# Kernel tuning notes

Hardware: AMD Instinct MI355X
Metric: run time of the kernel (lower is better)

## Reference

```python
import jax, jax.numpy as jnp
import numpy as np

HEADS = 4
LN_EPS = 1e-5

def layernorm(x, w, b):
    m = x.mean(-1, keepdims=True)
    v = ((x - m) ** 2).mean(-1, keepdims=True)
    return (x - m) * jax.lax.rsqrt(v + LN_EPS) * w + b

def conv3d(x, w, b, pad, dil=1, groups=1):
    out = jax.lax.conv_general_dilated(
        x, w, (1, 1, 1), [(pad, pad)] * 3,
        rhs_dilation=(dil, dil, dil),
        dimension_numbers=('NCDHW', 'OIDHW', 'NCDHW'),
        feature_group_count=groups)
    return out + b[None, :, None, None, None]

def trilinear_gather(x_flat, pz, py, px, D, H, W):
    # x_flat: [B,C,S]; pz/py/px: [B,S] fractional sample coords, zero padding outside
    z0f, y0f, x0f = jnp.floor(pz), jnp.floor(py), jnp.floor(px)
    wz, wy, wx = pz - z0f, py - y0f, px - x0f
    z0, y0, x0 = z0f.astype(jnp.int32), y0f.astype(jnp.int32), x0f.astype(jnp.int32)
    acc = jnp.zeros_like(x_flat)
    for dz in (0, 1):
        for dy in (0, 1):
            for dx in (0, 1):
                iz, iy, ix = z0 + dz, y0 + dy, x0 + dx
                cw = (wz if dz else 1.0 - wz) * (wy if dy else 1.0 - wy) * (wx if dx else 1.0 - wx)
                valid = (iz >= 0) & (iz < D) & (iy >= 0) & (iy < H) & (ix >= 0) & (ix < W)
                idx = (jnp.clip(iz, 0, D - 1) * H + jnp.clip(iy, 0, H - 1)) * W + jnp.clip(ix, 0, W - 1)
                vals = jnp.take_along_axis(x_flat, idx[:, None, :], axis=2)
                acc = acc + vals * (cw * valid)[:, None, :]
    return acc

def deform_conv3d(x, off_w, off_b, w, b):
    # DeformConvPack: offsets from a regular 3x3x3 conv, then offset trilinear sampling + conv
    B, C, D, H, W = x.shape
    K = 27
    offsets = conv3d(x, off_w, off_b, 1).reshape(B, K, 3, D * H * W)
    gz, gy, gx = jnp.indices((D, H, W))
    bz = gz.reshape(-1).astype(x.dtype)[None]
    by = gy.reshape(-1).astype(x.dtype)[None]
    bx = gx.reshape(-1).astype(x.dtype)[None]
    x_flat = x.reshape(B, C, -1)
    O = w.shape[0]
    wk = w.reshape(O, C, K)
    out = jnp.zeros((B, O, D * H * W), x.dtype)
    for k in range(K):  # fixed 27 kernel taps
        kz, ky, kx = k // 9, (k // 3) % 3, k % 3
        pz = bz + (kz - 1) + offsets[:, k, 0]
        py = by + (ky - 1) + offsets[:, k, 1]
        px = bx + (kx - 1) + offsets[:, k, 2]
        samp = trilinear_gather(x_flat, pz, py, px, D, H, W)  # [B,C,S]
        out = out + jnp.einsum('bcs,oc->bos', samp, wk[:, :, k])
    out = out + b[None, :, None]
    return out.reshape(B, O, D, H, W)

def forward(x, temperature, qkv_w, norm_w, norm_b, proj1_w, proj1_b, conv0_w, conv0_b,
            convsp_w, convsp_b, off_w, off_b, dcn_w, dcn_b, conv1_w, conv1_b,
            proj2_w, proj2_b, norm2_w, norm2_b, out_w, out_b, H, W, D):
    B, N, C = x.shape
    hd = C // HEADS
    qkv = (x @ qkv_w.T).reshape(B, N, 3, HEADS, hd).transpose(2, 0, 3, 1, 4)  # [3,B,h,N,hd]
    q = qkv[0].transpose(0, 1, 3, 2)  # [B,h,hd,N]
    k = qkv[1].transpose(0, 1, 3, 2)
    v = qkv[2].transpose(0, 1, 3, 2)
    q = q / jnp.maximum(jnp.sqrt((q * q).sum(-1, keepdims=True)), 1e-12)
    k = k / jnp.maximum(jnp.sqrt((k * k).sum(-1, keepdims=True)), 1e-12)
    attn = jnp.einsum('bhcn,bhdn->bhcd', q, k) * temperature[None]
    attn = jax.nn.softmax(attn, axis=-1)
    x_ca = jnp.einsum('bhcd,bhdn->bhcn', attn, v).transpose(0, 3, 1, 2).reshape(B, N, C)
    x_ca = layernorm(x_ca, norm_w, norm_b)
    x5 = x_ca.transpose(0, 2, 1).reshape(B, C, H, W, D)
    shortcut = x5
    y = jnp.einsum('bcxyz,oc->boxyz', x5, proj1_w) + proj1_b[None, :, None, None, None]
    y = jax.nn.gelu(y, approximate=False)
    u = y
    a = conv3d(y, conv0_w, conv0_b, 2, 1, C)      # depthwise k=5 pad=2
    a = conv3d(a, convsp_w, convsp_b, 9, 3, C)    # depthwise k=7 pad=9 dil=3
    a = deform_conv3d(a, off_w, off_b, dcn_w, dcn_b)
    a = jnp.einsum('bcxyz,oc->boxyz', a, conv1_w) + conv1_b[None, :, None, None, None]
    y = u * a
    y = jnp.einsum('bcxyz,oc->boxyz', y, proj2_w) + proj2_b[None, :, None, None, None]
    y = y + shortcut
    x_sa = y.reshape(B, C, N).transpose(0, 2, 1)           # lka returns [B,N,C]
    x_sa = x_sa.reshape(B, C, N).transpose(0, 2, 1)        # faithful torch reshape-after-permute
    x_sa = layernorm(x_sa, norm2_w, norm2_b)
    return x_sa @ out_w.T + out_b

def setup_inputs():
    key = jax.random.key(0)
    ks = jax.random.split(key, 12)
    B, C, H, W, D = 2, 64, 32, 32, 32
    N = H * W * D
    s = 0.02
    return dict(
        x=jax.random.normal(ks[0], (B, N, C), jnp.float32),
        temperature=jnp.ones((HEADS, 1, 1), jnp.float32),
        qkv_w=jax.random.normal(ks[1], (3 * C, C), jnp.float32) * s,
        norm_w=jnp.ones((C,), jnp.float32), norm_b=jnp.zeros((C,), jnp.float32),
        proj1_w=jax.random.normal(ks[2], (C, C), jnp.float32) * s,
        proj1_b=jnp.zeros((C,), jnp.float32),
        conv0_w=jax.random.normal(ks[3], (C, 1, 5, 5, 5), jnp.float32) * s,
        conv0_b=jnp.zeros((C,), jnp.float32),
        convsp_w=jax.random.normal(ks[4], (C, 1, 7, 7, 7), jnp.float32) * s,
        convsp_b=jnp.zeros((C,), jnp.float32),
        off_w=jax.random.normal(ks[5], (81, C, 3, 3, 3), jnp.float32) * 0.01,
        off_b=jnp.zeros((81,), jnp.float32),
        dcn_w=jax.random.normal(ks[6], (C, C, 3, 3, 3), jnp.float32) * s,
        dcn_b=jnp.zeros((C,), jnp.float32),
        conv1_w=jax.random.normal(ks[7], (C, C), jnp.float32) * s,
        conv1_b=jnp.zeros((C,), jnp.float32),
        proj2_w=jax.random.normal(ks[8], (C, C), jnp.float32) * s,
        proj2_b=jnp.zeros((C,), jnp.float32),
        norm2_w=jnp.ones((C,), jnp.float32), norm2_b=jnp.zeros((C,), jnp.float32),
        out_w=jax.random.normal(ks[9], (C, C), jnp.float32) * s,
        out_b=jnp.zeros((C,), jnp.float32),
        B_in=B, C_in=C, H=H, W=W, D=D,
    )

def reference(x, temperature, qkv_w, norm_w, norm_b, proj1_w, proj1_b, conv0_w, conv0_b,
              convsp_w, convsp_b, off_w, off_b, dcn_w, dcn_b, conv1_w, conv1_b,
              proj2_w, proj2_b, norm2_w, norm2_b, out_w, out_b, B_in, C_in, H, W, D):
    return forward(x, temperature, qkv_w, norm_w, norm_b, proj1_w, proj1_b, conv0_w, conv0_b,
                   convsp_w, convsp_b, off_w, off_b, dcn_w, dcn_b, conv1_w, conv1_b,
                   proj2_w, proj2_b, norm2_w, norm2_b, out_w, out_b, H, W, D)
```

## Files before the change

### kernel.cpp

```cpp
#include <hip/hip_runtime.h>
#include <hip/hip_bf16.h>

#define S 32768
#define BUFN (2*64*32768)

typedef __bf16 v8bf __attribute__((ext_vector_type(8)));
typedef float v4f __attribute__((ext_vector_type(4)));
typedef int v4i __attribute__((ext_vector_type(4)));

__device__ __forceinline__ ushort f2b(float f) {
  union { float f; unsigned u; } v; v.f = f;
  unsigned r = (v.u + 0x7fffu + ((v.u >> 16) & 1u)) >> 16;
  return (ushort)r;
}
__device__ __forceinline__ float b2f(ushort h) {
  union { unsigned u; float f; } v; v.u = ((unsigned)h) << 16;
  return v.f;
}
__device__ __forceinline__ float u2f(unsigned u) {
  union { unsigned u; float f; } v; v.u = u;
  return v.f;
}

__global__ void k_wt(const float* __restrict__ offw, const float* __restrict__ dcnw,
                     const float* __restrict__ qkvw, const float* __restrict__ p1w,
                     ushort* __restrict__ wt_off16, ushort* __restrict__ wt_dcn16,
                     ushort* __restrict__ qkv16, ushort* __restrict__ p1w16) {
  int i = blockIdx.x*256 + threadIdx.x;
  if (i < 27*96*64) {
    int c = i & 63, o = (i >> 6) % 96, t = i / 6144;
    wt_off16[i] = (o < 81) ? f2b(offw[o*1728 + c*27 + t]) : (ushort)0;
  }
  if (i < 27*64*64) {
    int c = i & 63, o = (i >> 6) & 63, k = i >> 12;
    wt_dcn16[i] = f2b(dcnw[(o*64 + c)*27 + k]);
  }
  if (i < 12288) qkv16[i] = f2b(qkvw[i]);
  if (i < 4096)  p1w16[i] = f2b(p1w[i]);
}

__global__ __launch_bounds__(256) void k_qkv(const float* __restrict__ x,
    const ushort* __restrict__ qkvw16, float* __restrict__ q,
    float* __restrict__ k, float* __restrict__ v) {
  int bi = blockIdx.x;
  int b = bi >> 9, tile = bi & 511;
  int tid = threadIdx.x;
  int lane = tid & 63, wv = tid >> 6;
  int si = lane & 15, rq = lane >> 4, q8 = rq << 3;
  int s = (tile << 6) + (wv << 4) + si;
  const float* xr = x + ((size_t)(b*S + s) << 6);
  float4 t0 = *(const float4*)(xr + q8);
  float4 t1 = *(const float4*)(xr + q8 + 4);
  float4 t2 = *(const float4*)(xr + q8 + 32);
  float4 t3 = *(const float4*)(xr + q8 + 36);
  float f0[8] = {t0.x,t0.y,t0.z,t0.w,t1.x,t1.y,t1.z,t1.w};
  float f1[8] = {t2.x,t2.y,t2.z,t2.w,t3.x,t3.y,t3.z,t3.w};
  v4i d0, d1;
#pragma unroll
  for (int m = 0; m < 4; m++) {
    d0[m] = (int)((unsigned)f2b(f0[2*m]) | ((unsigned)f2b(f0[2*m+1]) << 16));
    d1[m] = (int)((unsigned)f2b(f1[2*m]) | ((unsigned)f2b(f1[2*m+1]) << 16));
  }
  v8bf b0 = __builtin_bit_cast(v8bf, d0);
  v8bf b1 = __builtin_bit_cast(v8bf, d1);
  v4f acc[12];
#pragma unroll
  for (int t = 0; t < 12; t++) acc[t] = (v4f){0.f,0.f,0.f,0.f};
#pragma unroll
  for (int t = 0; t < 12; t++) {
    const ushort* ap = qkvw16 + (((t<<4) + si) << 6) + q8;
    v8bf a0 = *(const v8bf*)ap;
    v8bf a1 = *(const v8bf*)(ap + 32);
    acc[t] = __builtin_amdgcn_mfma_f32_16x16x32_bf16(a0, b0, acc[t], 0,0,0);
    acc[t] = __builtin_amdgcn_mfma_f32_16x16x32_bf16(a1, b1, acc[t], 0,0,0);
  }
#pragma unroll
  for (int t = 0; t < 12; t++) {
    float* dst = (t < 4) ? q : (t < 8 ? k : v);
    int chb = (t & 3) << 4;
#pragma unroll
    for (int r = 0; r < 4; r++) {
      int ch = chb + rq*4 + r;
      dst[((size_t)(b*64 + ch))*S + s] = acc[t][r];
    }
  }
}

__global__ __launch_bounds__(256) void k_rownorm(const float* __restrict__ q,
    const float* __restrict__ k, float* __restrict__ inv) {
  int row = blockIdx.x;
  const float* p = (row < 128) ? (q + (size_t)row*S) : (k + (size_t)(row-128)*S);
  const float4* p4 = (const float4*)p;
  float ss = 0.f;
  for (int i = threadIdx.x; i < S/4; i += 256) {
    float4 t = p4[i];
    ss += t.x*t.x + t.y*t.y + t.z*t.z + t.w*t.w;
  }
  __shared__ float red[256];
  red[threadIdx.x] = ss; __syncthreads();
  for (int st = 128; st > 0; st >>= 1) {
    if (threadIdx.x < st) red[threadIdx.x] += red[threadIdx.x+st];
    __syncthreads();
  }
  if (threadIdx.x == 0) inv[row] = 1.0f / fmaxf(sqrtf(red[0]), 1e-12f);
}

__global__ __launch_bounds__(256) void k_gram(const float* __restrict__ q,
    const float* __restrict__ k, float* __restrict__ gram) {
  __shared__ float qt[16][65], kt[16][65];
  int bi = blockIdx.x;
  int b = bi >> 7, h = (bi >> 5) & 3, chunk = bi & 31;
  int c = threadIdx.x >> 4, d = threadIdx.x & 15;
  const float* qb = q + ((size_t)(b*64 + h*16))*S;
  const float* kb = k + ((size_t)(b*64 + h*16))*S;
  int lr = threadIdx.x >> 4, lc = (threadIdx.x & 15) * 4;
  float acc = 0.f;
  for (int n0 = chunk*1024; n0 < chunk*1024 + 1024; n0 += 64) {
    float4 tq = *(const float4*)(qb + (size_t)lr*S + n0 + lc);
    float4 tk = *(const float4*)(kb + (size_t)lr*S + n0 + lc);
    __syncthreads();
    qt[lr][lc]=tq.x; qt[lr][lc+1]=tq.y; qt[lr][lc+2]=tq.z; qt[lr][lc+3]=tq.w;
    kt[lr][lc]=tk.x; kt[lr][lc+1]=tk.y; kt[lr][lc+2]=tk.z; kt[lr][lc+3]=tk.w;
    __syncthreads();
#pragma unroll
    for (int nn = 0; nn < 64; nn++) acc += qt[c][nn]*kt[d][nn];
  }
  atomicAdd(&gram[((b*4+h)*16+c)*16 + d], acc);
}

__global__ __launch_bounds__(256) void k_xca_ln(const float* __restrict__ v,
    const float* __restrict__ gram, const float* __restrict__ inv,
    const float* __restrict__ temp,
    const float* __restrict__ nw, const float* __restrict__ nb,
    float* __restrict__ x5) {
  __shared__ float at[1024];
  __shared__ float wsh[64], bsh[64];
  int gid = blockIdx.x*256 + threadIdx.x;
  int b = gid >> 15, n = gid & (S-1);
  int tid = threadIdx.x;
  if (tid < 64) {
    int h = tid >> 4, c = tid & 15;
    float iq = inv[b*64 + h*16 + c];
    float tp = temp[h];
    float l[16], m = -1e30f;
#pragma unroll
    for (int d = 0; d < 16; d++) {
      float vv = gram[((b*4+h)*16+c)*16 + d] * iq * inv[128 + b*64 + h*16 + d] * tp;
      l[d] = vv; m = fmaxf(m, vv);
    }
    float s = 0.f;
#pragma unroll
    for (int d = 0; d < 16; d++) { l[d] = expf(l[d]-m); s += l[d]; }
    float is = 1.0f / s;
#pragma unroll
    for (int d = 0; d < 16; d++) at[(h*16+c)*16 + d] = l[d]*is;
  } else if (tid < 128) {
    wsh[tid-64] = nw[tid-64]; bsh[tid-64] = nb[tid-64];
  }
  __syncthreads();
  const float* vb = v + (size_t)b*64*S + n;
  float vv[64];
#pragma unroll
  for (int ch = 0; ch < 64; ch++) vv[ch] = vb[(size_t)ch*S];
  float xc[64];
#pragma unroll
  for (int h = 0; h < 4; h++)
#pragma unroll
    for (int cc = 0; cc < 16; cc++) {
      float a = 0.f;
#pragma unroll
      for (int d = 0; d < 16; d++) a += at[(h*16+cc)*16 + d] * vv[h*16+d];
      xc[h*16+cc] = a;
    }
  float mean = 0.f;
#pragma unroll
  for (int ch = 0; ch < 64; ch++) mean += xc[ch];
  mean *= (1.0f/64.0f);
  float var = 0.f;
#pragma unroll
  for (int ch = 0; ch < 64; ch++) { float d = xc[ch]-mean; var += d*d; }
  var *= (1.0f/64.0f);
  float rs = rsqrtf(var + 1e-5f);
  float* xb = x5 + (size_t)b*64*S + n;
#pragma unroll
  for (int ch = 0; ch < 64; ch++)
    xb[(size_t)ch*S] = (xc[ch]-mean)*rs*wsh[ch] + bsh[ch];
}

__global__ __launch_bounds__(256) void k_proj1(const float* __restrict__ x5,
    const ushort* __restrict__ p1w16, const float* __restrict__ bias, float* __restrict__ u) {
  int bi = blockIdx.x;
  int b = bi >> 9, tile = bi & 511;
  int tid = threadIdx.x;
  int lane = tid & 63, wv = tid >> 6;
  int si = lane & 15, rq = lane >> 4, q8 = rq << 3;
  int s = (tile << 6) + (wv << 4) + si;
  const float* xb = x5 + ((size_t)b << 21) + s;
  float f0[8], f1[8];
#pragma unroll
  for (int j = 0; j < 8; j++) {
    f0[j] = xb[(size_t)(q8 + j) << 15];
    f1[j] = xb[(size_t)(32 + q8 + j) << 15];
  }
  v4i d0, d1;
#pragma unroll
  for (int m = 0; m < 4; m++) {
    d0[m] = (int)((unsigned)f2b(f0[2*m]) | ((unsigned)f2b(f0[2*m+1]) << 16));
    d1[m] = (int)((unsigned)f2b(f1[2*m]) | ((unsigned)f2b(f1[2*m+1]) << 16));
  }
  v8bf b0 = __builtin_bit_cast(v8bf, d0);
  v8bf b1 = __builtin_bit_cast(v8bf, d1);
  v4f acc[4];
#pragma unroll
  for (int t = 0; t < 4; t++) acc[t] = (v4f){0.f,0.f,0.f,0.f};
#pragma unroll
  for (int t = 0; t < 4; t++) {
    const ushort* ap = p1w16 + (((t<<4) + si) << 6) + q8;
    v8bf a0 = *(const v8bf*)ap;
    v8bf a1 = *(const v8bf*)(ap + 32);
    acc[t] = __builtin_amdgcn_mfma_f32_16x16x32_bf16(a0, b0, acc[t], 0,0,0);
    acc[t] = __builtin_amdgcn_mfma_f32_16x16x32_bf16(a1, b1, acc[t], 0,0,0);
  }
  float* ub = u + ((size_t)b << 21) + s;
#pragma unroll
  for (int t = 0; t < 4; t++)
#pragma unroll
    for (int r = 0; r < 4; r++) {
      int ch = (t << 4) + rq*4 + r;
      float a = acc[t][r] + bias[ch];
      float g = 0.5f*a*(1.0f + erff(a*0.70710678118654752f));
      ub[(size_t)ch << 15] = g;
    }
}

__global__ __launch_bounds__(256) void k_conv0(const float* __restrict__ in,
    const float* __restrict__ w, const float* __restrict__ bias, ushort* __restrict__ out) {
  __shared__ ushort tile[5*32*40];
  __shared__ float wsh[128];
  int bi = blockIdx.x;
  int z = bi & 31, c = (bi >> 5) & 63, b = bi >> 11;
  const float* ib = in + ((size_t)(b*64+c) << 15);
  for (int i = threadIdx.x; i < 800; i += 256)
    ((int4*)tile)[i] = make_int4(0,0,0,0);
  if (threadIdx.x < 125) wsh[threadIdx.x] = w[c*125 + threadIdx.x];
  __syncthreads();
  for (int i = threadIdx.x; i < 5*1024; i += 256) {
    int dz = i >> 10, r = i & 1023;
    int zg = z + dz - 2;
    if (zg >= 0 && zg < 32)
      tile[(dz*32 + (r >> 5))*40 + (r & 31) + 2] = f2b(ib[zg*1024 + r]);
  }
  __syncthreads();
  int y = threadIdx.x >> 3, x0 = (threadIdx.x & 7) << 2;
  float bv = bias[c];
  float acc[4] = {bv, bv, bv, bv};
  for (int dz = 0; dz < 5; dz++) {
#pragma unroll
    for (int dy = 0; dy < 5; dy++) {
      int yy = y + dy - 2;
      if (yy < 0 || yy >= 32) continue;
      const float* wp = &wsh[(dz*5+dy)*5];
      float wreg[5];
#pragma unroll
      for (int dx = 0; dx < 5; dx++) wreg[dx] = wp[dx];
      const ushort* rp = &tile[(dz*32+yy)*40 + x0];
      int2 rl = *(const int2*)rp;
      int2 rh = *(const int2*)(rp + 4);
      float row[8];
      row[0]=u2f(((unsigned)rl.x)<<16); row[1]=u2f(rl.x & 0xffff0000u);
      row[2]=u2f(((unsigned)rl.y)<<16); row[3]=u2f(rl.y & 0xffff0000u);
      row[4]=u2f(((unsigned)rh.x)<<16); row[5]=u2f(rh.x & 0xffff0000u);
      row[6]=u2f(((unsigned)rh.y)<<16); row[7]=u2f(rh.y & 0xffff0000u);
#pragma unroll
      for (int dx = 0; dx < 5; dx++)
#pragma unroll
        for (int j = 0; j < 4; j++)
          acc[j] += wreg[dx] * row[dx+j];
    }
  }
  ushort* ob = out + ((size_t)(b*64+c) << 15) + z*1024 + y*32 + x0;
  unsigned p0 = (unsigned)f2b(acc[0]) | ((unsigned)f2b(acc[1]) << 16);
  unsigned p1 = (unsigned)f2b(acc[2]) | ((unsigned)f2b(acc[3]) << 16);
  *(int2*)ob = make_int2((int)p0, (int)p1);
}

__global__ __launch_bounds__(256) void k_convsp(const ushort* __restrict__ in,
    const float* __restrict__ w, const float* __restrict__ bias, ushort* __restrict__ out) {
  __shared__ ushort tile[7*32*56];
  __shared__ float wsh[344];
  int bi = blockIdx.x;
  int z = bi & 31, c = (bi >> 5) & 63, b = bi >> 11;
  const ushort* ib = in + ((size_t)(b*64+c) << 15);
  for (int i = threadIdx.x; i < 1568; i += 256)
    ((int4*)tile)[i] = make_int4(0,0,0,0);
  for (int i = threadIdx.x; i < 343; i += 256) wsh[i] = w[c*343 + i];
  __syncthreads();
  for (int i = threadIdx.x; i < 7*1024; i += 256) {
    int t = i >> 10, r = i & 1023;
    int zg = z + 3*t - 9;
    if (zg >= 0 && zg < 32)
      tile[(t*32 + (r >> 5))*56 + (r & 31) + 9] = ib[zg*1024 + r];
  }
  __syncthreads();
  int y = threadIdx.x >> 3, x0 = (threadIdx.x & 7) << 2;
  float bv = bias[c];
  float acc[4] = {bv, bv, bv, bv};
  for (int t = 0; t < 7; t++) {
#pragma unroll
    for (int dy = 0; dy < 7; dy++) {
      int yy = y + 3*dy - 9;
      if (yy < 0 || yy >= 32) continue;
      const float* wp = &wsh[(t*7+dy)*7];
      float wreg[7];
#pragma unroll
      for (int dx = 0; dx < 7; dx++) wreg[dx] = wp[dx];
      const ushort* rp = &tile[(t*32+yy)*56 + x0];
      float row[24];
#pragma unroll
      for (int qq = 0; qq < 6; qq++) {
        int2 rv = *(const int2*)(rp + 4*qq);
        row[4*qq+0]=u2f(((unsigned)rv.x)<<16); row[4*qq+1]=u2f(rv.x & 0xffff0000u);
        row[4*qq+2]=u2f(((unsigned)rv.y)<<16); row[4*qq+3]=u2f(rv.y & 0xffff0000u);
      }
#pragma unroll
      for (int dx = 0; dx < 7; dx++)
#pragma unroll
        for (int j = 0; j < 4; j++)
          acc[j] += wreg[dx] * row[3*dx+j];
    }
  }
  ushort* ob = out + ((size_t)(b*64+c) << 15) + z*1024 + y*32 + x0;
  unsigned p0 = (unsigned)f2b(acc[0]) | ((unsigned)f2b(acc[1]) << 16);
  unsigned p1 = (unsigned)f2b(acc[2]) | ((unsigned)f2b(acc[3]) << 16);
  *(int2*)ob = make_int2((int)p0, (int)p1);
}

__global__ __launch_bounds__(256) void k_tr(const ushort* __restrict__ a2,
                                            ushort* __restrict__ a2t) {
  __shared__ ushort tile[64*66];
  int bi = blockIdx.x;
  int b = bi >> 9, chunk = bi & 511;
  int s0 = chunk << 6;
  const ushort* ib = a2 + ((size_t)b << 21) + s0;
#pragma unroll
  for (int i = 0; i < 16; i++) {
    int j = threadIdx.x + (i << 8);
    int c = j >> 6, sl = j & 63;
    tile[c*66 + sl] = ib[((size_t)c << 15) + sl];
  }
  __syncthreads();
  ushort* ob = a2t + ((size_t)b << 21) + ((size_t)s0 << 6);
#pragma unroll
  for (int i = 0; i < 16; i++) {
    int j = threadIdx.x + (i << 8);
    int sl = j >> 6, c = j & 63;
    ob[sl*64 + c] = tile[c*66 + sl];
  }
}

__global__ __launch_bounds__(256) void k_offconv(const ushort* __restrict__ a2t,
    const ushort* __restrict__ wt16, float* __restrict__ off) {
  int bi = blockIdx.x;
  int b = bi >> 9, tile = bi & 511;
  int s0 = tile << 6;
  int tid = threadIdx.x;
  int lane = tid & 63, wv = tid >> 6;
  int si = lane & 15, rq = lane >> 4, q8 = rq << 3;
  int sw = s0 + (wv << 4);
  int s_c = sw + si;
  int zc = s_c >> 10, yc = (s_c >> 5) & 31, xc = s_c & 31;
  const ushort* a2b = a2t + ((size_t)b << 21);
  v4f acc[6];
#pragma unroll
  for (int i = 0; i < 6; i++) acc[i] = (v4f){0.f,0.f,0.f,0.f};
  const v4i z4 = {0,0,0,0};
  for (int t = 0; t < 27; t++) {
    int kz = t/9, ky = (t/3)%3, kx = t%3;
    int zz = zc + kz - 1, yy = yc + ky - 1, xx = xc + kx - 1;
    bool ok = (zz>=0 && zz<32 && yy>=0 && yy<32 && xx>=0 && xx<32);
    v8bf b0 = __builtin_bit_cast(v8bf, z4);
    v8bf b1 = __builtin_bit_cast(v8bf, z4);
    if (ok) {
      const ushort* p = a2b + ((size_t)((zz<<10)+(yy<<5)+xx) << 6) + q8;
      b0 = *(const v8bf*)p;
      b1 = *(const v8bf*)(p + 32);
    }
    const ushort* wk = wt16 + t*6144;
#pragma unroll
    for (int ot = 0; ot < 6; ot++) {
      const ushort* ap = wk + (((ot<<4) + si) << 6) + q8;
      v8bf a0 = *(const v8bf*)ap;
      v8bf a1 = *(const v8bf*)(ap + 32);
      acc[ot] = __builtin_amdgcn_mfma_f32_16x16x32_bf16(a0, b0, acc[ot], 0,0,0);
      acc[ot] = __builtin_amdgcn_mfma_f32_16x16x32_bf16(a1, b1, acc[ot], 0,0,0);
    }
  }
#pragma unroll
  for (int ot = 0; ot < 6; ot++)
#pragma unroll
    for (int r = 0; r < 4; r++) {
      int o = ot*16 + rq*4 + r;
      if (o < 81)
        off[(((size_t)(b*81 + o)) << 15) + sw + si] = acc[ot][r];
    }
}

__global__ __launch_bounds__(256) void k_dcn(const ushort* __restrict__ a2t,
    const float* __restrict__ off, const float* __restrict__ off_b,
    const ushort* __restrict__ wt16, float* __restrict__ out) {
  __shared__ float ofs[81*66];
  __shared__ ushort scr[4][16*72];
  int bi = blockIdx.x;
  int b = bi >> 9, tile = bi & 511;
  int s0 = tile << 6;
  int tid = threadIdx.x;
  const float* offbase = off + (((size_t)(b*81)) << 15) + s0;
  for (int i = tid; i < 5184; i += 256) {
    int r = i >> 6, sl = i & 63;
    ofs[r*66 + sl] = offbase[((size_t)r << 15) + sl] + off_b[r];
  }
  __syncthreads();
  int lane = tid & 63, wv = tid >> 6;
  int sr = lane >> 3, cs = lane & 7;
  int si = lane & 15, rq = lane >> 4;
  int sw = s0 + (wv << 4);
  const ushort* a2b = a2t + ((size_t)b << 21);
  ushort* myscr = &scr[wv][0];
  int sA = sw + sr, sB = sw + 8 + sr;
  int zA = sA >> 10, yA = (sA >> 5) & 31, xA = sA & 31;
  int zB = sB >> 10, yB = (sB >> 5) & 31, xB = sB & 31;
  int slcA = (wv << 4) + sr, slcB = slcA + 8;
  v4f acc[4];
#pragma unroll
  for (int t = 0; t < 4; t++) acc[t] = (v4f){0.f,0.f,0.f,0.f};
  for (int k = 0; k < 27; k++) {
    int kz = k/9, ky = (k/3)%3, kx = k%3;
    int idxA[8], idxB[8];
    float wA[8], wB[8];
    {
      float pz = (float)(zA + kz - 1) + ofs[(3*k+0)*66 + slcA];
      float py = (float)(yA + ky - 1) + ofs[(3*k+1)*66 + slcA];
      float px = (float)(xA + kx - 1) + ofs[(3*k+2)*66 + slcA];
      float fz = floorf(pz), fy = floorf(py), fx = floorf(px);
      float wz = pz-fz, wy = py-fy, wx = px-fx;
      int z0 = (int)fz, y0 = (int)fy, x0 = (int)fx;
      int zi[2], yi[2], xi[2]; float zw[2], yw[2], xw[2];
#pragma unroll
      for (int d = 0; d < 2; d++) {
        int iz = z0 + d; zi[d] = min(max(iz,0),31) << 10;
        zw[d] = (iz >= 0 && iz < 32) ? (d ? wz : 1.f-wz) : 0.f;
        int iy = y0 + d; yi[d] = min(max(iy,0),31) << 5;
        yw[d] = (iy >= 0 && iy < 32) ? (d ? wy : 1.f-wy) : 0.f;
        int ix = x0 + d; xi[d] = min(max(ix,0),31);
        xw[d] = (ix >= 0 && ix < 32) ? (d ? wx : 1.f-wx) : 0.f;
      }
#pragma unroll
      for (int r = 0; r < 8; r++) {
        int dz = r >> 2, dy = (r >> 1) & 1, dx = r & 1;
        idxA[r] = zi[dz] + yi[dy] + xi[dx];
        wA[r] = zw[dz] * yw[dy] * xw[dx];
      }
    }
    {
      float pz = (float)(zB + kz - 1) + ofs[(3*k+0)*66 + slcB];
      float py = (float)(yB + ky - 1) + ofs[(3*k+1)*66 + slcB];
      float px = (float)(xB + kx - 1) + ofs[(3*k+2)*66 + slcB];
      float fz = floorf(pz), fy = floorf(py), fx = floorf(px);
      float wz = pz-fz, wy = py-fy, wx = px-fx;
      int z0 = (int)fz, y0 = (int)fy, x0 = (int)fx;
      int zi[2], yi[2], xi[2]; float zw[2], yw[2], xw[2];
#pragma unroll
      for (int d = 0; d < 2; d++) {
        int iz = z0 + d; zi[d] = min(max(iz,0),31) << 10;
        zw[d] = (iz >= 0 && iz < 32) ? (d ? wz : 1.f-wz) : 0.f;
        int iy = y0 + d; yi[d] = min(max(iy,0),31) << 5;
        yw[d] = (iy >= 0 && iy < 32) ? (d ? wy : 1.f-wy) : 0.f;
        int ix = x0 + d; xi[d] = min(max(ix,0),31);
        xw[d] = (ix >= 0 && ix < 32) ? (d ? wx : 1.f-wx) : 0.f;
      }
#pragma unroll
      for (int r = 0; r < 8; r++) {
        int dz = r >> 2, dy = (r >> 1) & 1, dx = r & 1;
        idxB[r] = zi[dz] + yi[dy] + xi[dx];
        wB[r] = zw[dz] * yw[dy] * xw[dx];
      }
    }
    v4i gA[8], gB[8];
#pragma unroll
    for (int r = 0; r < 8; r++)
      gA[r] = *(const v4i*)(a2b + ((size_t)idxA[r] << 6) + (cs << 3));
#pragma unroll
    for (int r = 0; r < 8; r++)
      gB[r] = *(const v4i*)(a2b + ((size_t)idxB[r] << 6) + (cs << 3));
    float faA[8], faB[8];
#pragma unroll
    for (int j = 0; j < 8; j++) { faA[j] = 0.f; faB[j] = 0.f; }
#pragma unroll
    for (int r = 0; r < 8; r++) {
      float wa = wA[r], wb = wB[r];
#pragma unroll
      for (int m = 0; m < 4; m++) {
        unsigned da = (unsigned)gA[r][m];
        faA[2*m]   += wa * u2f(da << 16);
        faA[2*m+1] += wa * u2f(da & 0xffff0000u);
        unsigned db = (unsigned)gB[r][m];
        faB[2*m]   += wb * u2f(db << 16);
        faB[2*m+1] += wb * u2f(db & 0xffff0000u);
      }
    }
    v4i dA, dB;
#pragma unroll
    for (int m = 0; m < 4; m++) {
      unsigned l0 = (__float_as_uint(faA[2*m])   + 0x8000u) >> 16;
      unsigned h0 = (__float_as_uint(faA[2*m+1]) + 0x8000u) & 0xffff0000u;
      dA[m] = (int)(l0 | h0);
      unsigned l1 = (__float_as_uint(faB[2*m])   + 0x8000u) >> 16;
      unsigned h1 = (__float_as_uint(faB[2*m+1]) + 0x8000u) & 0xffff0000u;
      dB[m] = (int)(l1 | h1);
    }
    *(v4i*)&myscr[sr*72 + (cs << 3)]       = dA;
    *(v4i*)&myscr[(8+sr)*72 + (cs << 3)]   = dB;
    v8bf bf0 = *(const v8bf*)&myscr[si*72 + (rq << 3)];
    v8bf bf1 = *(const v8bf*)&myscr[si*72 + 32 + (rq << 3)];
    const ushort* wk = wt16 + (k << 12);
#pragma unroll
    for (int ot = 0; ot < 4; ot++) {
      const ushort* ap = wk + (((ot<<4) + si) << 6) + (rq << 3);
      v8bf a0 = *(const v8bf*)ap;
      v8bf a1 = *(const v8bf*)(ap + 32);
      acc[ot] = __builtin_amdgcn_mfma_f32_16x16x32_bf16(a0, bf0, acc[ot], 0,0,0);
      acc[ot] = __builtin_amdgcn_mfma_f32_16x16x32_bf16(a1, bf1, acc[ot], 0,0,0);
    }
  }
#pragma unroll
  for (int ot = 0; ot < 4; ot++)
#pragma unroll
    for (int r = 0; r < 4; r++) {
      int o = (ot << 4) + rq*4 + r;
      out[(((size_t)(b*64 + o)) << 15) + sw + si] = acc[ot][r];
    }
}

__global__ __launch_bounds__(256) void k_fuse2(const float* __restrict__ dcn0,
    const float* __restrict__ dcn_b, const float* __restrict__ c1w,
    const float* __restrict__ c1b, const float* __restrict__ u,
    const float* __restrict__ p2w, const float* __restrict__ p2b,
    const float* __restrict__ x5, float* __restrict__ y2) {
  __shared__ float w1[4096], w2[4096];
  __shared__ float b1[64], b2[64], db[64];
  int gid = blockIdx.x*256 + threadIdx.x;
  for (int i = threadIdx.x; i < 4096; i += 256) { w1[i] = c1w[i]; w2[i] = p2w[i]; }
  if (threadIdx.x < 64) {
    b1[threadIdx.x]=c1b[threadIdx.x]; b2[threadIdx.x]=p2b[threadIdx.x];
    db[threadIdx.x]=dcn_b[threadIdx.x];
  }
  __syncthreads();
  int b = gid >> 15, n = gid & (S-1);
  const float* dbp0 = dcn0 + (size_t)b*64*S + n;
  float dv[64];
#pragma unroll
  for (int c = 0; c < 64; c++)
    dv[c] = dbp0[(size_t)c*S] + db[c];
  const float* ub = u + (size_t)b*64*S + n;
  float m[64];
  for (int o = 0; o < 64; o++) {
    const float4* w4 = (const float4*)&w1[o*64];
    float a = b1[o];
#pragma unroll
    for (int c4 = 0; c4 < 16; c4++) {
      float4 wv4 = w4[c4];
      a += dv[4*c4]*wv4.x + dv[4*c4+1]*wv4.y + dv[4*c4+2]*wv4.z + dv[4*c4+3]*wv4.w;
    }
    m[o] = ub[(size_t)o*S] * a;
  }
  const float* sb = x5 + (size_t)b*64*S + n;
  float* yb = y2 + (size_t)b*64*S + n;
  for (int o = 0; o < 64; o++) {
    const float4* w4 = (const float4*)&w2[o*64];
    float a = b2[o];
#pragma unroll
    for (int c4 = 0; c4 < 16; c4++) {
      float4 wv4 = w4[c4];
      a += m[4*c4]*wv4.x + m[4*c4+1]*wv4.y + m[4*c4+2]*wv4.z + m[4*c4+3]*wv4.w;
    }
    yb[(size_t)o*S] = a + sb[(size_t)o*S];
  }
}

__global__ __launch_bounds__(256) void k_final(const float* __restrict__ y2,
    const float* __restrict__ n2w, const float* __restrict__ n2b,
    const float* __restrict__ ow, const float* __restrict__ ob, float* __restrict__ out) {
  __shared__ float wsh[4096];
  __shared__ float nw[64], nb[64], obs[64];
  int bi = blockIdx.x;
  int b = bi >> 7; int mg = (bi >> 4) & 7; int r0 = (bi & 15)*4;
  for (int i = threadIdx.x; i < 4096; i += 256) wsh[i] = ow[i];
  if (threadIdx.x < 64) {
    nw[threadIdx.x]=n2w[threadIdx.x]; nb[threadIdx.x]=n2b[threadIdx.x];
    obs[threadIdx.x]=ob[threadIdx.x];
  }
  __syncthreads();
  int mi = threadIdx.x & 63, rg = threadIdx.x >> 6;
  int r = r0 + rg;
  int m = mg*64 + mi;
  int n = m*64 + r;
  const float* yb = y2 + ((size_t)(b*64+r))*S + m;
  float v[64];
#pragma unroll
  for (int c = 0; c < 64; c++) v[c] = yb[(size_t)c*512];
  float mean = 0.f;
#pragma unroll
  for (int c = 0; c < 64; c++) mean += v[c];
  mean *= (1.0f/64.0f);
  float var = 0.f;
#pragma unroll
  for (int c = 0; c < 64; c++) { float d = v[c]-mean; var += d*d; }
  var *= (1.0f/64.0f);
  float rs = rsqrtf(var + 1e-5f);
#pragma unroll
  for (int c = 0; c < 64; c++) v[c] = (v[c]-mean)*rs*nw[c] + nb[c];
  float* orow = out + ((size_t)b*S + n)*64;
  for (int o4 = 0; o4 < 16; o4++) {
    const float4* w0 = (const float4*)&wsh[(o4*4+0)*64];
    const float4* w1 = (const float4*)&wsh[(o4*4+1)*64];
    const float4* w2 = (const float4*)&wsh[(o4*4+2)*64];
    const float4* w3 = (const float4*)&wsh[(o4*4+3)*64];
    float t0=obs[o4*4+0], t1=obs[o4*4+1], t2=obs[o4*4+2], t3=obs[o4*4+3];
#pragma unroll
    for (int c4 = 0; c4 < 16; c4++) {
      float4 a0 = w0[c4], a1 = w1[c4], a2 = w2[c4], a3 = w3[c4];
      float v0 = v[4*c4], v1 = v[4*c4+1], v2 = v[4*c4+2], v3 = v[4*c4+3];
      t0 += a0.x*v0 + a0.y*v1 + a0.z*v2 + a0.w*v3;
      t1 += a1.x*v0 + a1.y*v1 + a1.z*v2 + a1.w*v3;
      t2 += a2.x*v0 + a2.y*v1 + a2.z*v2 + a2.w*v3;
      t3 += a3.x*v0 + a3.y*v1 + a3.z*v2 + a3.w*v3;
    }
    float4 a; a.x=t0; a.y=t1; a.z=t2; a.w=t3;
    ((float4*)orow)[o4] = a;
  }
}

extern "C" void kernel_launch(void* const* d_in, const int* in_sizes, int n_in,
                              void* d_out, int out_size, void* d_ws, size_t ws_size,
                              hipStream_t stream) {
  const float* x      = (const float*)d_in[0];
  const float* temp   = (const float*)d_in[1];
  const float* qkv_w  = (const float*)d_in[2];
  const float* norm_w = (const float*)d_in[3];
  const float* norm_b = (const float*)d_in[4];
  const float* p1w    = (const float*)d_in[5];
  const float* p1b    = (const float*)d_in[6];
  const float* c0w    = (const float*)d_in[7];
  const float* c0b    = (const float*)d_in[8];
  const float* cspw   = (const float*)d_in[9];
  const float* cspb   = (const float*)d_in[10];
  const float* offw   = (const float*)d_in[11];
  const float* offb   = (const float*)d_in[12];
  const float* dcnw   = (const float*)d_in[13];
  const float* dcnb   = (const float*)d_in[14];
  const float* c1w    = (const float*)d_in[15];
  const float* c1b    = (const float*)d_in[16];
  const float* p2w    = (const float*)d_in[17];
  const float* p2b    = (const float*)d_in[18];
  const float* n2w    = (const float*)d_in[19];
  const float* n2b    = (const float*)d_in[20];
  const float* outw   = (const float*)d_in[21];
  const float* outb   = (const float*)d_in[22];
  float* out = (float*)d_out;

  float* Wa  = (float*)d_ws;
  float* Wb  = Wa + BUFN;
  float* Wc  = Wb + BUFN;
  float* OFF = Wc + BUFN;
  float* SM  = OFF + (size_t)2*81*S;
  float* SM_inv  = SM;
  float* SM_gram = SM + 256;
  ushort* WT_OFF16 = (ushort*)(SM + 4352);
  ushort* WT_DCN16 = WT_OFF16 + 165888;
  ushort* QKV16    = WT_DCN16 + 110592;
  ushort* P1W16    = QKV16 + 12288;
  float* vbuf = out;
  ushort* A1_16 = (ushort*)d_out;
  ushort* A2_16 = (ushort*)Wc;
  ushort* a2t = (ushort*)d_out;

  hipMemsetAsync(SM, 0, 4352*sizeof(float), stream);
  k_wt     <<<648, 256, 0, stream>>>(offw, dcnw, qkv_w, p1w, WT_OFF16, WT_DCN16, QKV16, P1W16);

  k_qkv    <<<1024,256, 0, stream>>>(x, QKV16, Wa, Wb, vbuf);
  k_rownorm<<<256, 256, 0, stream>>>(Wa, Wb, SM_inv);
  k_gram   <<<256, 256, 0, stream>>>(Wa, Wb, SM_gram);
  k_xca_ln <<<256, 256, 0, stream>>>(vbuf, SM_gram, SM_inv, temp, norm_w, norm_b, Wa);
  k_proj1  <<<1024,256, 0, stream>>>(Wa, P1W16, p1b, Wb);
  k_conv0  <<<4096,256, 0, stream>>>(Wb, c0w, c0b, A1_16);
  k_convsp <<<4096,256, 0, stream>>>(A1_16, cspw, cspb, A2_16);
  k_tr     <<<1024,256, 0, stream>>>(A2_16, a2t);
  k_offconv<<<1024,256, 0, stream>>>(a2t, WT_OFF16, OFF);
  k_dcn    <<<1024,256, 0, stream>>>(a2t, OFF, offb, WT_DCN16, Wc);
  k_fuse2  <<<256, 256, 0, stream>>>(Wc, dcnb, c1w, c1b, Wb, p2w, p2b, Wa, OFF);
  k_final  <<<256, 256, 0, stream>>>(OFF, n2w, n2b, outw, outb, out);
}
```

Before: 791.7 us.

## Move gram and fuse2 channel matmuls onto bf16 MFMA

```diff
diff --git a/kernel.cpp b/kernel.cpp
--- a/kernel.cpp
+++ b/kernel.cpp
@@ -21,11 +21,20 @@
   union { unsigned u; float f; } v; v.u = u;
   return v.f;
 }
+__device__ __forceinline__ v8bf pack8(const float* f) {
+  v4i d;
+#pragma unroll
+  for (int m = 0; m < 4; m++)
+    d[m] = (int)((unsigned)f2b(f[2*m]) | ((unsigned)f2b(f[2*m+1]) << 16));
+  return __builtin_bit_cast(v8bf, d);
+}
 
 __global__ void k_wt(const float* __restrict__ offw, const float* __restrict__ dcnw,
                      const float* __restrict__ qkvw, const float* __restrict__ p1w,
+                     const float* __restrict__ c1w, const float* __restrict__ p2w,
                      ushort* __restrict__ wt_off16, ushort* __restrict__ wt_dcn16,
-                     ushort* __restrict__ qkv16, ushort* __restrict__ p1w16) {
+                     ushort* __restrict__ qkv16, ushort* __restrict__ p1w16,
+                     ushort* __restrict__ c1w16, ushort* __restrict__ p2w16) {
   int i = blockIdx.x*256 + threadIdx.x;
   if (i < 27*96*64) {
     int c = i & 63, o = (i >> 6) % 96, t = i / 6144;
@@ -36,7 +45,11 @@
     wt_dcn16[i] = f2b(dcnw[(o*64 + c)*27 + k]);
   }
   if (i < 12288) qkv16[i] = f2b(qkvw[i]);
-  if (i < 4096)  p1w16[i] = f2b(p1w[i]);
+  if (i < 4096) {
+    p1w16[i] = f2b(p1w[i]);
+    c1w16[i] = f2b(c1w[i]);
+    p2w16[i] = f2b(p2w[i]);
+  }
 }
 
 __global__ __launch_bounds__(256) void k_qkv(const float* __restrict__ x,
@@ -55,14 +68,8 @@
   float4 t3 = *(const float4*)(xr + q8 + 36);
   float f0[8] = {t0.x,t0.y,t0.z,t0.w,t1.x,t1.y,t1.z,t1.w};
   float f1[8] = {t2.x,t2.y,t2.z,t2.w,t3.x,t3.y,t3.z,t3.w};
-  v4i d0, d1;
-#pragma unroll
-  for (int m = 0; m < 4; m++) {
-    d0[m] = (int)((unsigned)f2b(f0[2*m]) | ((unsigned)f2b(f0[2*m+1]) << 16));
-    d1[m] = (int)((unsigned)f2b(f1[2*m]) | ((unsigned)f2b(f1[2*m+1]) << 16));
-  }
-  v8bf b0 = __builtin_bit_cast(v8bf, d0);
-  v8bf b1 = __builtin_bit_cast(v8bf, d1);
+  v8bf b0 = pack8(f0);
+  v8bf b1 = pack8(f1);
   v4f acc[12];
 #pragma unroll
   for (int t = 0; t < 12; t++) acc[t] = (v4f){0.f,0.f,0.f,0.f};
@@ -107,25 +114,33 @@
 
 __global__ __launch_bounds__(256) void k_gram(const float* __restrict__ q,
     const float* __restrict__ k, float* __restrict__ gram) {
-  __shared__ float qt[16][65], kt[16][65];
-  int bi = blockIdx.x;
-  int b = bi >> 7, h = (bi >> 5) & 3, chunk = bi & 31;
-  int c = threadIdx.x >> 4, d = threadIdx.x & 15;
-  const float* qb = q + ((size_t)(b*64 + h*16))*S;
-  const float* kb = k + ((size_t)(b*64 + h*16))*S;
-  int lr = threadIdx.x >> 4, lc = (threadIdx.x & 15) * 4;
-  float acc = 0.f;
-  for (int n0 = chunk*1024; n0 < chunk*1024 + 1024; n0 += 64) {
-    float4 tq = *(const float4*)(qb + (size_t)lr*S + n0 + lc);
-    float4 tk = *(const float4*)(kb + (size_t)lr*S + n0 + lc);
-    __syncthreads();
-    qt[lr][lc]=tq.x; qt[lr][lc+1]=tq.y; qt[lr][lc+2]=tq.z; qt[lr][lc+3]=tq.w;
-    kt[lr][lc]=tk.x; kt[lr][lc+1]=tk.y; kt[lr][lc+2]=tk.z; kt[lr][lc+3]=tk.w;
-    __syncthreads();
-#pragma unroll
-    for (int nn = 0; nn < 64; nn++) acc += qt[c][nn]*kt[d][nn];
-  }
-  atomicAdd(&gram[((b*4+h)*16+c)*16 + d], acc);
+  int bi = blockIdx.x;
+  int b = bi >> 8, h = (bi >> 6) & 3, chunk = bi & 63;
+  int tid = threadIdx.x;
+  int lane = tid & 63, wv = tid >> 6;
+  int si = lane & 15, rq = lane >> 4, q8 = rq << 3;
+  const float* qb = q + ((size_t)(b*64 + h*16 + si))*S;
+  const float* kb = k + ((size_t)(b*64 + h*16 + si))*S;
+  int n0 = chunk*512 + wv*128;
+  v4f acc = (v4f){0.f,0.f,0.f,0.f};
+#pragma unroll
+  for (int st = 0; st < 4; st++) {
+    int n = n0 + st*32 + q8;
+    float4 qa = *(const float4*)(qb + n);
+    float4 qc = *(const float4*)(qb + n + 4);
+    float4 ka = *(const float4*)(kb + n);
+    float4 kc = *(const float4*)(kb + n + 4);
+    float fq[8] = {qa.x,qa.y,qa.z,qa.w,qc.x,qc.y,qc.z,qc.w};
+    float fk[8] = {ka.x,ka.y,ka.z,ka.w,kc.x,kc.y,kc.z,kc.w};
+    v8bf a0 = pack8(fq);
+    v8bf b0 = pack8(fk);
+    acc = __builtin_amdgcn_mfma_f32_16x16x32_bf16(a0, b0, acc, 0,0,0);
+  }
+#pragma unroll
+  for (int r = 0; r < 4; r++) {
+    int c = rq*4 + r;
+    atomicAdd(&gram[((b*4+h)*16 + c)*16 + si], acc[r]);
+  }
 }
 
 __global__ __launch_bounds__(256) void k_xca_ln(const float* __restrict__ v,
@@ -202,14 +217,8 @@
     f0[j] = xb[(size_t)(q8 + j) << 15];
     f1[j] = xb[(size_t)(32 + q8 + j) << 15];
   }
-  v4i d0, d1;
-#pragma unroll
-  for (int m = 0; m < 4; m++) {
-    d0[m] = (int)((unsigned)f2b(f0[2*m]) | ((unsigned)f2b(f0[2*m+1]) << 16));
-    d1[m] = (int)((unsigned)f2b(f1[2*m]) | ((unsigned)f2b(f1[2*m+1]) << 16));
-  }
-  v8bf b0 = __builtin_bit_cast(v8bf, d0);
-  v8bf b1 = __builtin_bit_cast(v8bf, d1);
+  v8bf b0 = pack8(f0);
+  v8bf b1 = pack8(f1);
   v4f acc[4];
 #pragma unroll
   for (int t = 0; t < 4; t++) acc[t] = (v4f){0.f,0.f,0.f,0.f};
@@ -542,49 +551,69 @@
 }
 
 __global__ __launch_bounds__(256) void k_fuse2(const float* __restrict__ dcn0,
-    const float* __restrict__ dcn_b, const float* __restrict__ c1w,
+    const float* __restrict__ dcn_b, const ushort* __restrict__ c1w16,
     const float* __restrict__ c1b, const float* __restrict__ u,
-    const float* __restrict__ p2w, const float* __restrict__ p2b,
+    const ushort* __restrict__ p2w16, const float* __restrict__ p2b,
     const float* __restrict__ x5, float* __restrict__ y2) {
-  __shared__ float w1[4096], w2[4096];
-  __shared__ float b1[64], b2[64], db[64];
-  int gid = blockIdx.x*256 + threadIdx.x;
-  for (int i = threadIdx.x; i < 4096; i += 256) { w1[i] = c1w[i]; w2[i] = p2w[i]; }
-  if (threadIdx.x < 64) {
-    b1[threadIdx.x]=c1b[threadIdx.x]; b2[threadIdx.x]=p2b[threadIdx.x];
-    db[threadIdx.x]=dcn_b[threadIdx.x];
-  }
-  __syncthreads();
-  int b = gid >> 15, n = gid & (S-1);
-  const float* dbp0 = dcn0 + (size_t)b*64*S + n;
-  float dv[64];
-#pragma unroll
-  for (int c = 0; c < 64; c++)
-    dv[c] = dbp0[(size_t)c*S] + db[c];
-  const float* ub = u + (size_t)b*64*S + n;
-  float m[64];
-  for (int o = 0; o < 64; o++) {
-    const float4* w4 = (const float4*)&w1[o*64];
-    float a = b1[o];
-#pragma unroll
-    for (int c4 = 0; c4 < 16; c4++) {
-      float4 wv4 = w4[c4];
-      a += dv[4*c4]*wv4.x + dv[4*c4+1]*wv4.y + dv[4*c4+2]*wv4.z + dv[4*c4+3]*wv4.w;
-    }
-    m[o] = ub[(size_t)o*S] * a;
-  }
-  const float* sb = x5 + (size_t)b*64*S + n;
-  float* yb = y2 + (size_t)b*64*S + n;
-  for (int o = 0; o < 64; o++) {
-    const float4* w4 = (const float4*)&w2[o*64];
-    float a = b2[o];
-#pragma unroll
-    for (int c4 = 0; c4 < 16; c4++) {
-      float4 wv4 = w4[c4];
-      a += m[4*c4]*wv4.x + m[4*c4+1]*wv4.y + m[4*c4+2]*wv4.z + m[4*c4+3]*wv4.w;
-    }
-    yb[(size_t)o*S] = a + sb[(size_t)o*S];
-  }
+  __shared__ ushort scr[4][16*72];
+  int bi = blockIdx.x;
+  int b = bi >> 9, tile = bi & 511;
+  int tid = threadIdx.x;
+  int lane = tid & 63, wv = tid >> 6;
+  int si = lane & 15, rq = lane >> 4, q8 = rq << 3;
+  int s = (tile << 6) + (wv << 4) + si;
+  ushort* myscr = &scr[wv][0];
+  const float* db = dcn0 + ((size_t)b << 21) + s;
+  float f0[8], f1[8];
+#pragma unroll
+  for (int j = 0; j < 8; j++) {
+    f0[j] = db[(size_t)(q8 + j) << 15]      + dcn_b[q8 + j];
+    f1[j] = db[(size_t)(32 + q8 + j) << 15] + dcn_b[32 + q8 + j];
+  }
+  v8bf b0 = pack8(f0);
+  v8bf b1 = pack8(f1);
+  v4f acc1[4];
+#pragma unroll
+  for (int t = 0; t < 4; t++) acc1[t] = (v4f){0.f,0.f,0.f,0.f};
+#pragma unroll
+  for (int t = 0; t < 4; t++) {
+    const ushort* ap = c1w16 + (((t<<4) + si) << 6) + q8;
+    v8bf a0 = *(const v8bf*)ap;
+    v8bf a1 = *(const v8bf*)(ap + 32);
+    acc1[t] = __builtin_amdgcn_mfma_f32_16x16x32_bf16(a0, b0, acc1[t], 0,0,0);
+    acc1[t] = __builtin_amdgcn_mfma_f32_16x16x32_bf16(a1, b1, acc1[t], 0,0,0);
+  }
+  const float* ub = u + ((size_t)b << 21) + s;
+#pragma unroll
+  for (int t = 0; t < 4; t++)
+#pragma unroll
+    for (int r = 0; r < 4; r++) {
+      int o = (t << 4) + rq*4 + r;
+      float m = ub[(size_t)o << 15] * (acc1[t][r] + c1b[o]);
+      myscr[si*72 + o] = f2b(m);
+    }
+  v8bf m0 = *(const v8bf*)&myscr[si*72 + q8];
+  v8bf m1 = *(const v8bf*)&myscr[si*72 + 32 + q8];
+  v4f acc2[4];
+#pragma unroll
+  for (int t = 0; t < 4; t++) acc2[t] = (v4f){0.f,0.f,0.f,0.f};
+#pragma unroll
+  for (int t = 0; t < 4; t++) {
+    const ushort* ap = p2w16 + (((t<<4) + si) << 6) + q8;
+    v8bf a0 = *(const v8bf*)ap;
+    v8bf a1 = *(const v8bf*)(ap + 32);
+    acc2[t] = __builtin_amdgcn_mfma_f32_16x16x32_bf16(a0, m0, acc2[t], 0,0,0);
+    acc2[t] = __builtin_amdgcn_mfma_f32_16x16x32_bf16(a1, m1, acc2[t], 0,0,0);
+  }
+  const float* sb = x5 + ((size_t)b << 21) + s;
+  float* yb = y2 + ((size_t)b << 21) + s;
+#pragma unroll
+  for (int t = 0; t < 4; t++)
+#pragma unroll
+    for (int r = 0; r < 4; r++) {
+      int o = (t << 4) + rq*4 + r;
+      yb[(size_t)o << 15] = acc2[t][r] + p2b[o] + sb[(size_t)o << 15];
+    }
 }
 
 __global__ __launch_bounds__(256) void k_final(const float* __restrict__ y2,
@@ -679,17 +708,20 @@
   ushort* WT_DCN16 = WT_OFF16 + 165888;
   ushort* QKV16    = WT_DCN16 + 110592;
   ushort* P1W16    = QKV16 + 12288;
+  ushort* C1W16    = P1W16 + 4096;
+  ushort* P2W16    = C1W16 + 4096;
   float* vbuf = out;
   ushort* A1_16 = (ushort*)d_out;
   ushort* A2_16 = (ushort*)Wc;
   ushort* a2t = (ushort*)d_out;
 
   hipMemsetAsync(SM, 0, 4352*sizeof(float), stream);
-  k_wt     <<<648, 256, 0, stream>>>(offw, dcnw, qkv_w, p1w, WT_OFF16, WT_DCN16, QKV16, P1W16);
+  k_wt     <<<648, 256, 0, stream>>>(offw, dcnw, qkv_w, p1w, c1w, p2w,
+                                     WT_OFF16, WT_DCN16, QKV16, P1W16, C1W16, P2W16);
 
   k_qkv    <<<1024,256, 0, stream>>>(x, QKV16, Wa, Wb, vbuf);
   k_rownorm<<<256, 256, 0, stream>>>(Wa, Wb, SM_inv);
-  k_gram   <<<256, 256, 0, stream>>>(Wa, Wb, SM_gram);
+  k_gram   <<<512, 256, 0, stream>>>(Wa, Wb, SM_gram);
   k_xca_ln <<<256, 256, 0, stream>>>(vbuf, SM_gram, SM_inv, temp, norm_w, norm_b, Wa);
   k_proj1  <<<1024,256, 0, stream>>>(Wa, P1W16, p1b, Wb);
   k_conv0  <<<4096,256, 0, stream>>>(Wb, c0w, c0b, A1_16);
@@ -697,6 +729,6 @@
   k_tr     <<<1024,256, 0, stream>>>(A2_16, a2t);
   k_offconv<<<1024,256, 0, stream>>>(a2t, WT_OFF16, OFF);
   k_dcn    <<<1024,256, 0, stream>>>(a2t, OFF, offb, WT_DCN16, Wc);
-  k_fuse2  <<<256, 256, 0, stream>>>(Wc, dcnb, c1w, c1b, Wb, p2w, p2b, Wa, OFF);
+  k_fuse2  <<<1024,256, 0, stream>>>(Wc, dcnb, C1W16, c1b, Wb, P2W16, p2b, Wa, OFF);
   k_final  <<<256, 256, 0, stream>>>(OFF, n2w, n2b, outw, outb, out);
 }
```

Result: faster. 733.8 us (-7.3%).
